# Performance work log

Hardware: AMD Instinct MI355X
Metric: run time of the kernel (lower is better)

## Reference

```python
import jax, jax.numpy as jnp
import numpy as np

N, D = 8192, 128

def setup_inputs() -> dict:
    key = jax.random.key(0)
    kq, kk, kv = jax.random.split(key, 3)
    query = jax.random.normal(kq, (N, D), dtype=jnp.float32)
    key_t = jax.random.normal(kk, (N, D), dtype=jnp.float32)
    value = jax.random.normal(kv, (N, D), dtype=jnp.float32)
    return {"query": query, "key": key_t, "value": value}

def reference(query, key, value):
    # FlashAttention-2 online softmax over blocks is mathematically exact
    # softmax attention: out = softmax(Q K^T / sqrt(d)) V, no mask.
    d = query.shape[-1]
    scale = 1.0 / jnp.sqrt(jnp.asarray(d, dtype=query.dtype))
    scores = jnp.einsum('qd,kd->qk', query, key) * scale  # [n, n]
    probs = jax.nn.softmax(scores, axis=-1)
    return jnp.einsum('qk,kd->qd', probs, value)  # [n, d]
```

## Files before the change

### kernel.cpp

```cpp
#include <hip/hip_runtime.h>
#include <hip/hip_bf16.h>

#define ATTN_N 8192
#define ATTN_D 128
#define TKEYS 64
#define NTILES (ATTN_N / TKEYS)
#define TILE_ELEMS (TKEYS * ATTN_D)
#define QROWS 64
#define SPLITK 4
#define KTPB (NTILES / SPLITK)

typedef __bf16 bf16_t;
typedef bf16_t bf16x2 __attribute__((ext_vector_type(2)));
typedef bf16_t bf16x8 __attribute__((ext_vector_type(8)));
typedef float f32x4 __attribute__((ext_vector_type(4)));

#if __has_builtin(__builtin_amdgcn_exp2f)
#define EXP2(x) __builtin_amdgcn_exp2f(x)
#else
#define EXP2(x) __expf((x) * 0.6931471805599453f)
#endif

__device__ __forceinline__ void dma16(const bf16_t* g, bf16_t* l) {
  __builtin_amdgcn_global_load_lds(
      (const __attribute__((address_space(1))) void*)g,
      (__attribute__((address_space(3))) void*)l, 16, 0, 0);
}

__global__ void prep_kernel(const float* __restrict__ q,
                            const float* __restrict__ k,
                            const float* __restrict__ v,
                            bf16_t* __restrict__ qb,
                            bf16_t* __restrict__ kswz,
                            bf16_t* __restrict__ vtswz) {
  __shared__ bf16_t tile[64][72];
  const int bk = blockIdx.x;
  const int bd = blockIdx.y;
  const int t = threadIdx.x;
  const float sc = 0.12751744f;

  const int row_l = t >> 2;
  const int key = bk * 64 + row_l;

#pragma unroll
  for (int u = 0; u < 2; ++u) {
    const int j = bd * 8 + (t & 3) * 2 + u;
    const float4* qs = (const float4*)(q + (size_t)key * ATTN_D + j * 8);
    const float4* ks = (const float4*)(k + (size_t)key * ATTN_D + j * 8);
    float4 a0 = qs[0], a1 = qs[1];
    float4 b0 = ks[0], b1 = ks[1];
    bf16x8 qo, ko;
    qo[0] = (bf16_t)(a0.x * sc); qo[1] = (bf16_t)(a0.y * sc);
    qo[2] = (bf16_t)(a0.z * sc); qo[3] = (bf16_t)(a0.w * sc);
    qo[4] = (bf16_t)(a1.x * sc); qo[5] = (bf16_t)(a1.y * sc);
    qo[6] = (bf16_t)(a1.z * sc); qo[7] = (bf16_t)(a1.w * sc);
    ko[0] = (bf16_t)b0.x; ko[1] = (bf16_t)b0.y;
    ko[2] = (bf16_t)b0.z; ko[3] = (bf16_t)b0.w;
    ko[4] = (bf16_t)b1.x; ko[5] = (bf16_t)b1.y;
    ko[6] = (bf16_t)b1.z; ko[7] = (bf16_t)b1.w;
    *(bf16x8*)(qb + (size_t)key * ATTN_D + j * 8) = qo;
    *(bf16x8*)(kswz + (size_t)key * ATTN_D + ((j ^ (key & 15)) * 8)) = ko;
  }

  {
    const float* src = v + (size_t)key * ATTN_D + bd * 64 + (t & 3) * 16;
#pragma unroll
    for (int u = 0; u < 4; ++u) {
      float4 a = ((const float4*)src)[u];
      tile[row_l][(t & 3) * 16 + u * 4 + 0] = (bf16_t)a.x;
      tile[row_l][(t & 3) * 16 + u * 4 + 1] = (bf16_t)a.y;
      tile[row_l][(t & 3) * 16 + u * 4 + 2] = (bf16_t)a.z;
      tile[row_l][(t & 3) * 16 + u * 4 + 3] = (bf16_t)a.w;
    }
  }
  __syncthreads();
  {
    const int d_l = t >> 2;
    const int d = bd * 64 + d_l;
#pragma unroll
    for (int u = 0; u < 2; ++u) {
      const int j = (t & 3) * 2 + u;
      bf16x8 o;
#pragma unroll
      for (int i = 0; i < 8; ++i) {
        const int kl_ = 32 * (j >> 2) + 4 * (j & 3) + (i >> 1) + 16 * (i & 1);
        o[i] = tile[kl_][d_l];
      }
      *(bf16x8*)(vtswz + (size_t)bk * TILE_ELEMS + d * TKEYS +
                 ((j ^ (d & 7)) * 8)) = o;
    }
  }
}

__global__ __launch_bounds__(512, 4) void flash_attn_kernel(
    const bf16_t* __restrict__ qb, const bf16_t* __restrict__ kswz,
    const bf16_t* __restrict__ vtswz, float* __restrict__ partO,
    float* __restrict__ partL) {
  __shared__ __align__(16) bf16_t KV[2][2][TILE_ELEMS];
  __shared__ __align__(16) bf16_t Ps[8][16][40];
  __shared__ float cmb[8][16];
  float* Ob = (float*)&KV[0][0][0];

  const int t = threadIdx.x;
  const int w = t >> 6;
  const int lane = t & 63;
  const int quad = lane >> 4;
  const int col = lane & 15;
  const int rowQ = w & 3;
  const int keyQ = w >> 2;
  const int blk = blockIdx.x;
  const int qg = blk >> 2;
  const int kh = blk & 3;
  const int q0 = qg * QROWS;
  const int ktbase = kh * KTPB;
  const int stg = ((blk >> 3) & 3) * 8;

  int offK[4][2], offV[8];
#pragma unroll
  for (int c = 0; c < 4; ++c)
#pragma unroll
    for (int ni = 0; ni < 2; ++ni)
      offK[c][ni] = (keyQ * 32 + ni * 16 + col) * ATTN_D +
                    (((c * 4 + quad) ^ col) * 8);
#pragma unroll
  for (int ds = 0; ds < 8; ++ds)
    offV[ds] = (ds * 16 + col) * TKEYS + (((keyQ * 4 + quad) ^ (col & 7)) * 8);

  bf16x8 aq[4];
  {
    const int row = q0 + rowQ * 16 + col;
#pragma unroll
    for (int c = 0; c < 4; ++c)
      aq[c] = *(const bf16x8*)(qb + (size_t)row * ATTN_D + c * 32 + quad * 8);
  }

  f32x4 oacc[8];
#pragma unroll
  for (int i = 0; i < 8; ++i) oacc[i] = (f32x4){0.f, 0.f, 0.f, 0.f};
  float l_part[4] = {0.f, 0.f, 0.f, 0.f};

  {
    const int kt = ktbase + (stg & (KTPB - 1));
    const bf16_t* kg = kswz + (size_t)kt * TILE_ELEMS + t * 8;
    const bf16_t* vg = vtswz + (size_t)kt * TILE_ELEMS + t * 8;
#pragma unroll
    for (int u = 0; u < 2; ++u) {
      dma16(kg + u * 4096, &KV[0][0][t * 8 + u * 4096]);
      dma16(vg + u * 4096, &KV[0][1][t * 8 + u * 4096]);
    }
  }
  __syncthreads();

  for (int it = 0; it < KTPB; ++it) {
    const int buf = it & 1;
    if (it + 1 < KTPB) {
      const int nt = ktbase + ((stg + it + 1) & (KTPB - 1));
      const bf16_t* kg = kswz + (size_t)nt * TILE_ELEMS + t * 8;
      const bf16_t* vg = vtswz + (size_t)nt * TILE_ELEMS + t * 8;
      bf16_t* kl = &KV[buf ^ 1][0][t * 8];
      bf16_t* vl = &KV[buf ^ 1][1][t * 8];
#pragma unroll
      for (int u = 0; u < 2; ++u) {
        dma16(kg + u * 4096, kl + u * 4096);
        dma16(vg + u * 4096, vl + u * 4096);
      }
    }
    const bf16_t* Kb = KV[buf][0];
    const bf16_t* Vb = KV[buf][1];

    f32x4 s0 = (f32x4){0.f, 0.f, 0.f, 0.f};
    f32x4 s1 = (f32x4){0.f, 0.f, 0.f, 0.f};
    __builtin_amdgcn_s_setprio(1);
#pragma unroll
    for (int c = 0; c < 4; ++c) {
      bf16x8 b0 = *(const bf16x8*)(Kb + offK[c][0]);
      bf16x8 b1 = *(const bf16x8*)(Kb + offK[c][1]);
      s0 = __builtin_amdgcn_mfma_f32_16x16x32_bf16(aq[c], b0, s0, 0, 0, 0);
      s1 = __builtin_amdgcn_mfma_f32_16x16x32_bf16(aq[c], b1, s1, 0, 0, 0);
    }
    __builtin_amdgcn_s_setprio(0);

#pragma unroll
    for (int r = 0; r < 4; ++r) {
      float p0 = EXP2(s0[r]);
      float p1 = EXP2(s1[r]);
      l_part[r] += p0 + p1;
      *(bf16x2*)&Ps[w][quad * 4 + r][col * 2] = (bf16x2){(bf16_t)p0, (bf16_t)p1};
    }

    bf16x8 ap = *(const bf16x8*)&Ps[w][col][quad * 8];
    __builtin_amdgcn_s_setprio(1);
#pragma unroll
    for (int ds = 0; ds < 8; ++ds) {
      bf16x8 bv = *(const bf16x8*)(Vb + offV[ds]);
      oacc[ds] = __builtin_amdgcn_mfma_f32_16x16x32_bf16(ap, bv, oacc[ds], 0, 0, 0);
    }
    __builtin_amdgcn_s_setprio(0);
    __syncthreads();
  }

#pragma unroll
  for (int r = 0; r < 4; ++r) {
    float v = l_part[r];
#pragma unroll
    for (int off = 1; off < 16; off <<= 1)
      v += __shfl_xor(v, off, 64);
    if (col == 0) cmb[w][quad * 4 + r] = v;
  }
  __syncthreads();
  if (t < QROWS) {
    const int rq = t >> 4, rl = t & 15;
    partL[(size_t)blk * QROWS + t] = cmb[rq][rl] + cmb[4 + rq][rl];
  }

#pragma unroll
  for (int p = 0; p < 2; ++p) {
    if (keyQ == p) {
#pragma unroll
      for (int ds = 0; ds < 8; ++ds)
#pragma unroll
        for (int r = 0; r < 4; ++r) {
          const int row = rowQ * 16 + quad * 4 + r;
          if (p == 0)
            Ob[row * 132 + ds * 16 + col] = oacc[ds][r];
          else
            Ob[row * 132 + ds * 16 + col] += oacc[ds][r];
        }
    }
    __syncthreads();
  }

  {
    float* dst = partO + (size_t)blk * (QROWS * ATTN_D);
    const int row = t >> 3;
    const int c0 = (t & 7) * 16;
#pragma unroll
    for (int u = 0; u < 4; ++u) {
      float4 vv = *(float4*)&Ob[row * 132 + c0 + u * 4];
      *(float4*)(dst + row * ATTN_D + c0 + u * 4) = vv;
    }
  }
}

__global__ void merge_kernel(const float* __restrict__ partO,
                             const float* __restrict__ partL,
                             float* __restrict__ out) {
  const int idx = blockIdx.x * blockDim.x + threadIdx.x;
  const int row = idx >> 5;
  const int gi = row >> 6;
  const int rl = row & 63;
  const int li = rl * 32 + (idx & 31);
  const float4* p0 = (const float4*)(partO + (size_t)(4 * gi + 0) * (QROWS * ATTN_D));
  const float4* p1 = (const float4*)(partO + (size_t)(4 * gi + 1) * (QROWS * ATTN_D));
  const float4* p2 = (const float4*)(partO + (size_t)(4 * gi + 2) * (QROWS * ATTN_D));
  const float4* p3 = (const float4*)(partO + (size_t)(4 * gi + 3) * (QROWS * ATTN_D));
  const float invL = 1.0f / (partL[(size_t)(4 * gi + 0) * QROWS + rl] +
                             partL[(size_t)(4 * gi + 1) * QROWS + rl] +
                             partL[(size_t)(4 * gi + 2) * QROWS + rl] +
                             partL[(size_t)(4 * gi + 3) * QROWS + rl]);
  float4 a = p0[li], b = p1[li], c = p2[li], d = p3[li], o;
  o.x = (a.x + b.x + c.x + d.x) * invL;
  o.y = (a.y + b.y + c.y + d.y) * invL;
  o.z = (a.z + b.z + c.z + d.z) * invL;
  o.w = (a.w + b.w + c.w + d.w) * invL;
  ((float4*)out)[idx] = o;
}

extern "C" void kernel_launch(void* const* d_in, const int* in_sizes, int n_in,
                              void* d_out, int out_size, void* d_ws, size_t ws_size,
                              hipStream_t stream) {
  const float* q = (const float*)d_in[0];
  const float* k = (const float*)d_in[1];
  const float* v = (const float*)d_in[2];
  float* out = (float*)d_out;

  bf16_t* qb = (bf16_t*)d_ws;
  bf16_t* kswz = qb + (size_t)ATTN_N * ATTN_D;
  bf16_t* vtswz = kswz + (size_t)ATTN_N * ATTN_D;
  float* partO = (float*)(vtswz + (size_t)ATTN_N * ATTN_D);
  float* partL = partO + (size_t)512 * QROWS * ATTN_D;

  prep_kernel<<<dim3(ATTN_N / 64, 2), 256, 0, stream>>>(q, k, v, qb, kswz, vtswz);
  flash_attn_kernel<<<512, 512, 0, stream>>>(qb, kswz, vtswz, partO, partL);
  merge_kernel<<<(ATTN_N * ATTN_D / 4) / 256, 256, 0, stream>>>(partO, partL, out);
}
```

Before: 116.6 us.

## Use 32-key tiles, 128-row blocks, 8-way key split with 4-stage DMA pipeline

Shrinks key tiles to 32 and gives each of the 8 waves its own 16 query rows over the whole tile, which removes the LDS cross-wave reduction of partial outputs. It deepens prefetch to a 4-buffer ring with explicit vmcnt waits and raw barriers in place of full syncthreads, and raises the key split to 8 with a matching merge. Partial outputs are now written straight from registers with strided stores. The cost is twice the partial-output traffic in the merge step, plus more barriers per key because the tiles are smaller.

```diff
diff --git a/kernel.cpp b/kernel.cpp
--- a/kernel.cpp
+++ b/kernel.cpp
@@ -3,12 +3,13 @@
 
 #define ATTN_N 8192
 #define ATTN_D 128
-#define TKEYS 64
+#define TKEYS 32
 #define NTILES (ATTN_N / TKEYS)
 #define TILE_ELEMS (TKEYS * ATTN_D)
-#define QROWS 64
-#define SPLITK 4
+#define QROWS 128
+#define SPLITK 8
 #define KTPB (NTILES / SPLITK)
+#define NBUF 4
 
 typedef __bf16 bf16_t;
 typedef bf16_t bf16x2 __attribute__((ext_vector_type(2)));
@@ -77,17 +78,17 @@
   {
     const int d_l = t >> 2;
     const int d = bd * 64 + d_l;
-#pragma unroll
-    for (int u = 0; u < 2; ++u) {
-      const int j = (t & 3) * 2 + u;
+    const int cq = t & 3;
+#pragma unroll
+    for (int h = 0; h < 2; ++h) {
       bf16x8 o;
 #pragma unroll
-      for (int i = 0; i < 8; ++i) {
-        const int kl_ = 32 * (j >> 2) + 4 * (j & 3) + (i >> 1) + 16 * (i & 1);
-        o[i] = tile[kl_][d_l];
+      for (int j = 0; j < 8; ++j) {
+        const int kl_ = h * 32 + cq * 4 + (j >> 1) + 16 * (j & 1);
+        o[j] = tile[kl_][d_l];
       }
-      *(bf16x8*)(vtswz + (size_t)bk * TILE_ELEMS + d * TKEYS +
-                 ((j ^ (d & 7)) * 8)) = o;
+      *(bf16x8*)(vtswz + (size_t)(2 * bk + h) * TILE_ELEMS + d * TKEYS +
+                 ((cq ^ ((d >> 1) & 3)) * 8)) = o;
     }
   }
 }
@@ -96,21 +97,17 @@
     const bf16_t* __restrict__ qb, const bf16_t* __restrict__ kswz,
     const bf16_t* __restrict__ vtswz, float* __restrict__ partO,
     float* __restrict__ partL) {
-  __shared__ __align__(16) bf16_t KV[2][2][TILE_ELEMS];
+  __shared__ __align__(16) bf16_t KV[NBUF][2][TILE_ELEMS];
   __shared__ __align__(16) bf16_t Ps[8][16][40];
-  __shared__ float cmb[8][16];
-  float* Ob = (float*)&KV[0][0][0];
 
   const int t = threadIdx.x;
   const int w = t >> 6;
   const int lane = t & 63;
   const int quad = lane >> 4;
   const int col = lane & 15;
-  const int rowQ = w & 3;
-  const int keyQ = w >> 2;
   const int blk = blockIdx.x;
-  const int qg = blk >> 2;
-  const int kh = blk & 3;
+  const int qg = blk >> 3;
+  const int kh = blk & 7;
   const int q0 = qg * QROWS;
   const int ktbase = kh * KTPB;
   const int stg = ((blk >> 3) & 3) * 8;
@@ -120,15 +117,14 @@
   for (int c = 0; c < 4; ++c)
 #pragma unroll
     for (int ni = 0; ni < 2; ++ni)
-      offK[c][ni] = (keyQ * 32 + ni * 16 + col) * ATTN_D +
-                    (((c * 4 + quad) ^ col) * 8);
+      offK[c][ni] = (ni * 16 + col) * ATTN_D + (((c * 4 + quad) ^ col) * 8);
 #pragma unroll
   for (int ds = 0; ds < 8; ++ds)
-    offV[ds] = (ds * 16 + col) * TKEYS + (((keyQ * 4 + quad) ^ (col & 7)) * 8);
+    offV[ds] = (ds * 16 + col) * TKEYS + ((quad ^ ((col >> 1) & 3)) * 8);
 
   bf16x8 aq[4];
   {
-    const int row = q0 + rowQ * 16 + col;
+    const int row = q0 + w * 16 + col;
 #pragma unroll
     for (int c = 0; c < 4; ++c)
       aq[c] = *(const bf16x8*)(qb + (size_t)row * ATTN_D + c * 32 + quad * 8);
@@ -139,31 +135,22 @@
   for (int i = 0; i < 8; ++i) oacc[i] = (f32x4){0.f, 0.f, 0.f, 0.f};
   float l_part[4] = {0.f, 0.f, 0.f, 0.f};
 
-  {
-    const int kt = ktbase + (stg & (KTPB - 1));
-    const bf16_t* kg = kswz + (size_t)kt * TILE_ELEMS + t * 8;
-    const bf16_t* vg = vtswz + (size_t)kt * TILE_ELEMS + t * 8;
-#pragma unroll
-    for (int u = 0; u < 2; ++u) {
-      dma16(kg + u * 4096, &KV[0][0][t * 8 + u * 4096]);
-      dma16(vg + u * 4096, &KV[0][1][t * 8 + u * 4096]);
-    }
-  }
-  __syncthreads();
+#pragma unroll
+  for (int pt = 0; pt < 3; ++pt) {
+    const int kt = ktbase + ((stg + pt) & (KTPB - 1));
+    dma16(kswz + (size_t)kt * TILE_ELEMS + t * 8, &KV[pt][0][t * 8]);
+    dma16(vtswz + (size_t)kt * TILE_ELEMS + t * 8, &KV[pt][1][t * 8]);
+  }
+  asm volatile("s_waitcnt vmcnt(4)" ::: "memory");
+  __builtin_amdgcn_s_barrier();
 
   for (int it = 0; it < KTPB; ++it) {
-    const int buf = it & 1;
-    if (it + 1 < KTPB) {
-      const int nt = ktbase + ((stg + it + 1) & (KTPB - 1));
-      const bf16_t* kg = kswz + (size_t)nt * TILE_ELEMS + t * 8;
-      const bf16_t* vg = vtswz + (size_t)nt * TILE_ELEMS + t * 8;
-      bf16_t* kl = &KV[buf ^ 1][0][t * 8];
-      bf16_t* vl = &KV[buf ^ 1][1][t * 8];
-#pragma unroll
-      for (int u = 0; u < 2; ++u) {
-        dma16(kg + u * 4096, kl + u * 4096);
-        dma16(vg + u * 4096, vl + u * 4096);
-      }
+    const int buf = it & (NBUF - 1);
+    if (it + 3 < KTPB) {
+      const int nt = ktbase + ((stg + it + 3) & (KTPB - 1));
+      const int nb = (it + 3) & (NBUF - 1);
+      dma16(kswz + (size_t)nt * TILE_ELEMS + t * 8, &KV[nb][0][t * 8]);
+      dma16(vtswz + (size_t)nt * TILE_ELEMS + t * 8, &KV[nb][1][t * 8]);
     }
     const bf16_t* Kb = KV[buf][0];
     const bf16_t* Vb = KV[buf][1];
@@ -196,7 +183,17 @@
       oacc[ds] = __builtin_amdgcn_mfma_f32_16x16x32_bf16(ap, bv, oacc[ds], 0, 0, 0);
     }
     __builtin_amdgcn_s_setprio(0);
-    __syncthreads();
+
+    if (it + 3 < KTPB) {
+      asm volatile("s_waitcnt vmcnt(4)" ::: "memory");
+      __builtin_amdgcn_s_barrier();
+    } else if (it + 2 < KTPB) {
+      asm volatile("s_waitcnt vmcnt(2)" ::: "memory");
+      __builtin_amdgcn_s_barrier();
+    } else if (it + 1 < KTPB) {
+      asm volatile("s_waitcnt vmcnt(0)" ::: "memory");
+      __builtin_amdgcn_s_barrier();
+    }
   }
 
 #pragma unroll
@@ -205,40 +202,17 @@
 #pragma unroll
     for (int off = 1; off < 16; off <<= 1)
       v += __shfl_xor(v, off, 64);
-    if (col == 0) cmb[w][quad * 4 + r] = v;
-  }
-  __syncthreads();
-  if (t < QROWS) {
-    const int rq = t >> 4, rl = t & 15;
-    partL[(size_t)blk * QROWS + t] = cmb[rq][rl] + cmb[4 + rq][rl];
-  }
-
-#pragma unroll
-  for (int p = 0; p < 2; ++p) {
-    if (keyQ == p) {
-#pragma unroll
-      for (int ds = 0; ds < 8; ++ds)
-#pragma unroll
-        for (int r = 0; r < 4; ++r) {
-          const int row = rowQ * 16 + quad * 4 + r;
-          if (p == 0)
-            Ob[row * 132 + ds * 16 + col] = oacc[ds][r];
-          else
-            Ob[row * 132 + ds * 16 + col] += oacc[ds][r];
-        }
-    }
-    __syncthreads();
-  }
-
-  {
-    float* dst = partO + (size_t)blk * (QROWS * ATTN_D);
-    const int row = t >> 3;
-    const int c0 = (t & 7) * 16;
-#pragma unroll
-    for (int u = 0; u < 4; ++u) {
-      float4 vv = *(float4*)&Ob[row * 132 + c0 + u * 4];
-      *(float4*)(dst + row * ATTN_D + c0 + u * 4) = vv;
-    }
+    if (col == 0)
+      partL[(size_t)blk * QROWS + w * 16 + quad * 4 + r] = v;
+  }
+
+  {
+    float* dst = partO + ((size_t)blk * QROWS + w * 16) * ATTN_D;
+#pragma unroll
+    for (int ds = 0; ds < 8; ++ds)
+#pragma unroll
+      for (int r = 0; r < 4; ++r)
+        dst[(quad * 4 + r) * ATTN_D + ds * 16 + col] = oacc[ds][r];
   }
 }
 
@@ -247,22 +221,22 @@
                              float* __restrict__ out) {
   const int idx = blockIdx.x * blockDim.x + threadIdx.x;
   const int row = idx >> 5;
-  const int gi = row >> 6;
-  const int rl = row & 63;
+  const int gi = row >> 7;
+  const int rl = row & 127;
   const int li = rl * 32 + (idx & 31);
-  const float4* p0 = (const float4*)(partO + (size_t)(4 * gi + 0) * (QROWS * ATTN_D));
-  const float4* p1 = (const float4*)(partO + (size_t)(4 * gi + 1) * (QROWS * ATTN_D));
-  const float4* p2 = (const float4*)(partO + (size_t)(4 * gi + 2) * (QROWS * ATTN_D));
-  const float4* p3 = (const float4*)(partO + (size_t)(4 * gi + 3) * (QROWS * ATTN_D));
-  const float invL = 1.0f / (partL[(size_t)(4 * gi + 0) * QROWS + rl] +
-                             partL[(size_t)(4 * gi + 1) * QROWS + rl] +
-                             partL[(size_t)(4 * gi + 2) * QROWS + rl] +
-                             partL[(size_t)(4 * gi + 3) * QROWS + rl]);
-  float4 a = p0[li], b = p1[li], c = p2[li], d = p3[li], o;
-  o.x = (a.x + b.x + c.x + d.x) * invL;
-  o.y = (a.y + b.y + c.y + d.y) * invL;
-  o.z = (a.z + b.z + c.z + d.z) * invL;
-  o.w = (a.w + b.w + c.w + d.w) * invL;
+  float L = 0.f;
+  float4 acc = {0.f, 0.f, 0.f, 0.f};
+#pragma unroll
+  for (int i = 0; i < 8; ++i) {
+    const size_t b = (size_t)(8 * gi + i);
+    L += partL[b * QROWS + rl];
+    float4 a = ((const float4*)(partO + b * (QROWS * ATTN_D)))[li];
+    acc.x += a.x; acc.y += a.y; acc.z += a.z; acc.w += a.w;
+  }
+  const float invL = 1.0f / L;
+  float4 o;
+  o.x = acc.x * invL; o.y = acc.y * invL;
+  o.z = acc.z * invL; o.w = acc.w * invL;
   ((float4*)out)[idx] = o;
 }
 
```

After: 109.3 us. 6.2% less time.
